# Optimization experiments

Measured on AMD Instinct MI355X. Metric: run time of the kernel, lower is better.

Reference implementation:

```python
import jax, jax.numpy as jnp
import numpy as np
import math

N_KM = [64, 16]  # part_nums_hierarchical
SPATIAL = 891    # 11*9*9, hardcoded in the original reshape


def _make_im2cluster(C, K, seed):
    # random assignment but guarantee >=2 members per cluster (original code
    # indexes zs[0] and skips singleton clusters, but would crash on empties)
    rng = np.random.RandomState(seed)
    base = np.repeat(np.arange(K), 2)
    rest = rng.randint(0, K, size=C - base.size)
    return np.concatenate([base, rest]).astype(np.int64)


def setup_inputs() -> dict:
    key = jax.random.key(0)
    conv_features = jax.random.normal(key, (8, 4096, 11, 9, 9), dtype=jnp.float32)
    im2cluster_0 = jnp.asarray(_make_im2cluster(4096, 64, 1))
    im2cluster_1 = jnp.asarray(_make_im2cluster(4096, 16, 2))
    return {"conv_features": conv_features,
            "im2cluster_0": im2cluster_0,
            "im2cluster_1": im2cluster_1}


def _safe_norm(diff):
    # row-wise L2 norm, grad-safe at exactly-zero rows (row 0 is zs[0]-zs[0])
    sq = jnp.sum(diff * diff, axis=1)
    return jnp.where(sq > 0, jnp.sqrt(jnp.where(sq > 0, sq, 1.0)), 0.0)


def _hpro_loss(conv_features, im2clusters):
    bs, C = conv_features.shape[0], conv_features.shape[1]
    D = SPATIAL * bs
    x = conv_features.reshape(bs, C, SPATIAL)
    loss = jnp.float32(0.0)
    loss_node = jnp.float32(0.0)
    for m, K in enumerate(N_KM):
        im2c = np.asarray(im2clusters[m])  # constant indices -> concrete group sizes
        zs_m, conc_m = [], []
        for c in range(K):
            idx = np.nonzero(im2c == c)[0]
            # faithful torch reshape: [bs, n_c, 891] -> [n_c, 891*bs] (row-major)
            zs = x[:, idx, :].reshape(-1, D)
            n_c = zs.shape[0]
            norm_sum = jnp.sum(_safe_norm(zs - zs[0]))
            conc_m.append(norm_sum / (n_c * math.log(n_c + 10)))
            zs_m.append(zs)
        rs = jnp.stack([z[0] for z in zs_m], axis=1)  # [D, K] first-member reps
        for c in range(K):
            u1 = zs_m[c]
            if u1.shape[0] == 1:
                continue
            nom = jnp.sum(u1 * u1[0], axis=1) / conc_m[c]                     # [n_c]
            den = jax.scipy.special.logsumexp((u1 @ rs) / conc_m[c], axis=1)  # [n_c]
            loss = loss + (-(nom - den)).mean()
        if m == 0:
            loss_node = loss
    return loss_node / C, (loss - loss_node) / (len(N_KM) * C)


def reference(conv_features, im2cluster_0, im2cluster_1):
    return _hpro_loss(conv_features, [im2cluster_0, im2cluster_1])
```

## Files before the change

### kernel.cpp

```cpp
#include <hip/hip_runtime.h>
#include <math.h>

#define CCH 4096
#define SP 891

typedef __attribute__((ext_vector_type(8))) short short8;
typedef __attribute__((ext_vector_type(4))) float f32x4;

__device__ __forceinline__ unsigned int pack_bf2(float a, float b) {
  unsigned int ua = __builtin_bit_cast(unsigned int, a);
  unsigned int ub = __builtin_bit_cast(unsigned int, b);
  ua = (ua + 0x7fffu + ((ua >> 16) & 1u)) >> 16;
  ub = (ub + 0x7fffu + ((ub >> 16) & 1u)) >> 16;
  return ua | (ub << 16);
}

__global__ void k_setup(const int* __restrict__ im0, const int* __restrict__ im1,
                        int* cnt0, int* off0, int* cnt1, int* off1,
                        int* mem0, int* mem1, int* rs0, int* rs1) {
  int cb = blockIdx.x;
  int level = (cb >= 64) ? 1 : 0;
  int c = level ? cb - 64 : cb;
  const int* im = level ? im1 : im0;
  int* members = level ? mem1 : mem0;
  int* rs = level ? rs1 : rs0;
  int lane = threadIdx.x;
  int lt = 0;
  for (int ch = lane; ch < CCH; ch += 64) lt += (im[ch] < c) ? 1 : 0;
  for (int o = 32; o; o >>= 1) lt += __shfl_xor(lt, o, 64);
  int base = lt;
  int cnt = 0;
  for (int chunk = 0; chunk < CCH; chunk += 64) {
    int ch = chunk + lane;
    bool m = (im[ch] == c);
    unsigned long long mk = __ballot(m);
    int pos = __popcll(mk & ((1ull << lane) - 1ull));
    if (m) members[base + cnt + pos] = ch;
    cnt += __popcll(mk);
  }
  int n = cnt;
  if (lane == 0) {
    if (level) { cnt1[c] = n; off1[c] = base; }
    else       { cnt0[c] = n; off0[c] = base; }
  }
  __syncthreads();
  for (int r = lane; r < n; r += 64) {
    #pragma unroll
    for (int q = 0; q < 8; q++) {
      int p = 8 * r + q;
      int b = p / n, j = p - b * n;
      rs[(size_t)(base + r) * 8 + q] = b * CCH + members[base + j];
    }
  }
}

__global__ void k_brep(const float* __restrict__ X,
    const int* __restrict__ off0, const int* __restrict__ off1,
    const int* __restrict__ rs0, const int* __restrict__ rs1,
    uint4* __restrict__ Bfrag0, uint4* __restrict__ Bfrag1) {
  int gid = blockIdx.x * 4 + (threadIdx.x >> 6);
  int l = threadIdx.x & 63;
  int lrow = l & 15, hi = l >> 4;
  int level = (gid >= 32) ? 1 : 0;
  int q = level ? (gid - 32) : (gid >> 2);
  int ct = level ? 0 : (gid & 3);
  int cc = ct * 16 + lrow;
  int base = level ? off1[cc] : off0[cc];
  int sid = (level ? rs1 : rs0)[(size_t)base * 8 + q];
  const float* ap = X + (size_t)sid * SP + hi * 8;
  uint4* dst = (level ? Bfrag1 + (size_t)(q * 28) * 64
                      : Bfrag0 + (size_t)((q * 4 + ct) * 28) * 64) + l;
  #pragma unroll 3
  for (int kc = 0; kc < 27; kc++) {
    float4 fa0 = *(const float4*)(ap + kc * 32);
    float4 fa1 = *(const float4*)(ap + kc * 32 + 4);
    uint4 ua;
    ua.x = pack_bf2(fa0.x, fa0.y); ua.y = pack_bf2(fa0.z, fa0.w);
    ua.z = pack_bf2(fa1.x, fa1.y); ua.w = pack_bf2(fa1.z, fa1.w);
    dst[kc * 64] = ua;
  }
  {
    float4 fa0, fa1;
    if (hi == 3) {
      fa0 = make_float4(ap[864], ap[865], ap[866], 0.f);
      fa1 = make_float4(0.f, 0.f, 0.f, 0.f);
    } else {
      fa0 = *(const float4*)(ap + 864);
      fa1 = *(const float4*)(ap + 868);
    }
    uint4 ua;
    ua.x = pack_bf2(fa0.x, fa0.y); ua.y = pack_bf2(fa0.z, fa0.w);
    ua.z = pack_bf2(fa1.x, fa1.y); ua.w = pack_bf2(fa1.z, fa1.w);
    dst[27 * 64] = ua;
  }
}

__global__ __launch_bounds__(256) void k_gemm_all(const float* __restrict__ X,
    const int* __restrict__ rs0, const int* __restrict__ rs1,
    const uint4* __restrict__ Bfrag0, const uint4* __restrict__ Bfrag1,
    float* __restrict__ P8_0, float* __restrict__ P8_1, float* __restrict__ sn2) {
  const int q = blockIdx.y, tid = threadIdx.x;
  const int l = tid & 63, w = tid >> 6;
  const int lrow = l & 15, hi = l >> 4;
  if (blockIdx.x < 128) {
    const int wm = w & 1, wn = w >> 1;
    const int rowTile = blockIdx.x * 2 + wm;
    const int sid = rs0[(size_t)(rowTile * 16 + lrow) * 8 + q];
    const float* ap = X + (size_t)sid * SP + hi * 8;
    const uint4* bq0 = Bfrag0 + (size_t)((q * 4 + wn * 2) * 28) * 64 + l;
    const uint4* bq1 = Bfrag0 + (size_t)((q * 4 + wn * 2 + 1) * 28) * 64 + l;
    f32x4 acc0 = {0.f, 0.f, 0.f, 0.f}, acc1 = {0.f, 0.f, 0.f, 0.f};
    float s2 = 0.f;
    #pragma unroll 3
    for (int kc = 0; kc < 27; kc++) {
      float4 fa0 = *(const float4*)(ap + kc * 32);
      float4 fa1 = *(const float4*)(ap + kc * 32 + 4);
      uint4 ub0 = bq0[kc * 64];
      uint4 ub1 = bq1[kc * 64];
      uint4 ua;
      ua.x = pack_bf2(fa0.x, fa0.y); ua.y = pack_bf2(fa0.z, fa0.w);
      ua.z = pack_bf2(fa1.x, fa1.y); ua.w = pack_bf2(fa1.z, fa1.w);
      s2 += fa0.x * fa0.x + fa0.y * fa0.y + fa0.z * fa0.z + fa0.w * fa0.w
          + fa1.x * fa1.x + fa1.y * fa1.y + fa1.z * fa1.z + fa1.w * fa1.w;
      short8 a = __builtin_bit_cast(short8, ua);
      acc0 = __builtin_amdgcn_mfma_f32_16x16x32_bf16(a, __builtin_bit_cast(short8, ub0), acc0, 0, 0, 0);
      acc1 = __builtin_amdgcn_mfma_f32_16x16x32_bf16(a, __builtin_bit_cast(short8, ub1), acc1, 0, 0, 0);
    }
    {
      float4 fa0, fa1;
      if (hi == 3) {
        fa0 = make_float4(ap[864], ap[865], ap[866], 0.f);
        fa1 = make_float4(0.f, 0.f, 0.f, 0.f);
      } else {
        fa0 = *(const float4*)(ap + 864);
        fa1 = *(const float4*)(ap + 868);
      }
      uint4 ub0 = bq0[27 * 64];
      uint4 ub1 = bq1[27 * 64];
      uint4 ua;
      ua.x = pack_bf2(fa0.x, fa0.y); ua.y = pack_bf2(fa0.z, fa0.w);
      ua.z = pack_bf2(fa1.x, fa1.y); ua.w = pack_bf2(fa1.z, fa1.w);
      s2 += fa0.x * fa0.x + fa0.y * fa0.y + fa0.z * fa0.z + fa0.w * fa0.w
          + fa1.x * fa1.x + fa1.y * fa1.y + fa1.z * fa1.z + fa1.w * fa1.w;
      short8 a = __builtin_bit_cast(short8, ua);
      acc0 = __builtin_amdgcn_mfma_f32_16x16x32_bf16(a, __builtin_bit_cast(short8, ub0), acc0, 0, 0, 0);
      acc1 = __builtin_amdgcn_mfma_f32_16x16x32_bf16(a, __builtin_bit_cast(short8, ub1), acc1, 0, 0, 0);
    }
    #pragma unroll
    for (int r = 0; r < 4; r++) {
      int row = rowTile * 16 + hi * 4 + r;
      float* dst = P8_0 + ((size_t)q * CCH + row) * 64;
      dst[wn * 32 + lrow] = acc0[r];
      dst[wn * 32 + 16 + lrow] = acc1[r];
    }
    s2 += __shfl_xor(s2, 16, 64);
    s2 += __shfl_xor(s2, 32, 64);
    if (wn == 0 && hi == 0) sn2[sid] = s2;
  } else {
    const int bx = blockIdx.x - 128;
    const int rowTile = bx * 4 + w;
    const int sid = rs1[(size_t)(rowTile * 16 + lrow) * 8 + q];
    const float* ap = X + (size_t)sid * SP + hi * 8;
    const uint4* bq = Bfrag1 + (size_t)(q * 28) * 64 + l;
    f32x4 acc = {0.f, 0.f, 0.f, 0.f};
    #pragma unroll 3
    for (int kc = 0; kc < 27; kc++) {
      float4 fa0 = *(const float4*)(ap + kc * 32);
      float4 fa1 = *(const float4*)(ap + kc * 32 + 4);
      uint4 ub = bq[kc * 64];
      uint4 ua;
      ua.x = pack_bf2(fa0.x, fa0.y); ua.y = pack_bf2(fa0.z, fa0.w);
      ua.z = pack_bf2(fa1.x, fa1.y); ua.w = pack_bf2(fa1.z, fa1.w);
      acc = __builtin_amdgcn_mfma_f32_16x16x32_bf16(
          __builtin_bit_cast(short8, ua), __builtin_bit_cast(short8, ub), acc, 0, 0, 0);
    }
    {
      float4 fa0, fa1;
      if (hi == 3) {
        fa0 = make_float4(ap[864], ap[865], ap[866], 0.f);
        fa1 = make_float4(0.f, 0.f, 0.f, 0.f);
      } else {
        fa0 = *(const float4*)(ap + 864);
        fa1 = *(const float4*)(ap + 868);
      }
      uint4 ub = bq[27 * 64];
      uint4 ua;
      ua.x = pack_bf2(fa0.x, fa0.y); ua.y = pack_bf2(fa0.z, fa0.w);
      ua.z = pack_bf2(fa1.x, fa1.y); ua.w = pack_bf2(fa1.z, fa1.w);
      acc = __builtin_amdgcn_mfma_f32_16x16x32_bf16(
          __builtin_bit_cast(short8, ua), __builtin_bit_cast(short8, ub), acc, 0, 0, 0);
    }
    #pragma unroll
    for (int r = 0; r < 4; r++) {
      int row = rowTile * 16 + hi * 4 + r;
      P8_1[((size_t)q * CCH + row) * 16 + lrow] = acc[r];
    }
  }
}

template<int K>
__device__ __forceinline__ void fin_body(const float* __restrict__ P8,
    const float* __restrict__ sn2, const int* __restrict__ rs,
    const int* __restrict__ cnt, const int* __restrict__ off,
    double* __restrict__ clLoss, int c) {
  __shared__ float pcc[4096];
  __shared__ float red[256];
  __shared__ double redd[256];
  __shared__ float s_conc;
  const int n = cnt[c], base = off[c];
  const int tid = threadIdx.x;
  float rn0 = 0.f;
  #pragma unroll
  for (int qq = 0; qq < 8; qq++) rn0 += sn2[rs[(size_t)base * 8 + qq]];
  float t = 0.f;
  for (int r = tid; r < n; r += 256) {
    float pd = 0.f, rn = 0.f;
    #pragma unroll
    for (int qq = 0; qq < 8; qq++) {
      pd += P8[((size_t)qq * CCH + base + r) * K + c];
      rn += sn2[rs[(size_t)(base + r) * 8 + qq]];
    }
    pcc[r] = pd;
    if (r > 0) {
      float d2 = rn - 2.f * pd + rn0;
      t += (d2 > 0.f) ? sqrtf(d2) : 0.f;
    }
  }
  red[tid] = t; __syncthreads();
  for (int o = 128; o; o >>= 1) { if (tid < o) red[tid] += red[tid + o]; __syncthreads(); }
  if (tid == 0) s_conc = red[0] / ((float)n * logf((float)n + 10.f));
  __syncthreads();
  const float invc = 1.f / s_conc;
  const int wv = tid >> 6, lane = tid & 63;
  const int sub = (K == 64) ? 0 : (lane >> 4);
  const int cc = lane & (K - 1);
  constexpr int RPI = (K == 64) ? 4 : 16;
  double acc = 0.0;
  for (int r = wv * (RPI / 4) + sub; r < n; r += RPI) {
    float s = 0.f;
    #pragma unroll
    for (int qq = 0; qq < 8; qq++) s += P8[((size_t)qq * CCH + base + r) * K + cc];
    float lg = s * invc;
    float m = lg;
    #pragma unroll
    for (int o = K / 2; o; o >>= 1) m = fmaxf(m, __shfl_xor(m, o, K));
    float e = expf(lg - m);
    float se = e;
    #pragma unroll
    for (int o = K / 2; o; o >>= 1) se += __shfl_xor(se, o, K);
    if (cc == 0) acc += (double)(m + logf(se)) - (double)(pcc[r] * invc);
  }
  redd[tid] = acc; __syncthreads();
  for (int o = 128; o; o >>= 1) { if (tid < o) redd[tid] += redd[tid + o]; __syncthreads(); }
  if (tid == 0) clLoss[c] = redd[0] / (double)n;
}

__global__ __launch_bounds__(256) void k_fin_all(const float* __restrict__ P8_0,
    const float* __restrict__ P8_1, const float* __restrict__ sn2,
    const int* __restrict__ rs0, const int* __restrict__ rs1,
    const int* __restrict__ cnt0, const int* __restrict__ off0,
    const int* __restrict__ cnt1, const int* __restrict__ off1,
    double* __restrict__ cl0, double* __restrict__ cl1) {
  if (blockIdx.x < 64) fin_body<64>(P8_0, sn2, rs0, cnt0, off0, cl0, blockIdx.x);
  else                 fin_body<16>(P8_1, sn2, rs1, cnt1, off1, cl1, blockIdx.x - 64);
}

__global__ void k_final(const double* __restrict__ cl0, const double* __restrict__ cl1,
                        float* __restrict__ out) {
  if (threadIdx.x == 0) {
    double s0 = 0.0, s1 = 0.0;
    for (int i = 0; i < 64; i++) s0 += cl0[i];
    for (int i = 0; i < 16; i++) s1 += cl1[i];
    out[0] = (float)(s0 / 4096.0);
    out[1] = (float)(s1 / 8192.0);
  }
}

extern "C" void kernel_launch(void* const* d_in, const int* in_sizes, int n_in,
                              void* d_out, int out_size, void* d_ws, size_t ws_size,
                              hipStream_t stream) {
  const float* X = (const float*)d_in[0];
  const int* im0 = (const int*)d_in[1];
  const int* im1 = (const int*)d_in[2];
  float* out = (float*)d_out;

  char* w = (char*)d_ws;
  auto alloc = [&](size_t bytes) -> char* {
    char* p = w; w += (bytes + 255) & ~(size_t)255; return p;
  };
  int*    cnt0  = (int*)alloc(64 * 4);
  int*    off0  = (int*)alloc(64 * 4);
  int*    cnt1  = (int*)alloc(16 * 4);
  int*    off1  = (int*)alloc(16 * 4);
  int*    mem0  = (int*)alloc((size_t)CCH * 4);
  int*    mem1  = (int*)alloc((size_t)CCH * 4);
  int*    rs0   = (int*)alloc((size_t)CCH * 8 * 4);
  int*    rs1   = (int*)alloc((size_t)CCH * 8 * 4);
  float*  sn2   = (float*)alloc((size_t)8 * CCH * 4);
  uint4*  Bfrag0 = (uint4*)alloc((size_t)32 * 28 * 64 * 16);
  uint4*  Bfrag1 = (uint4*)alloc((size_t)8 * 28 * 64 * 16);
  float*  P8_0  = (float*)alloc((size_t)8 * CCH * 64 * 4);
  float*  P8_1  = (float*)alloc((size_t)8 * CCH * 16 * 4);
  double* cl0   = (double*)alloc(64 * 8);
  double* cl1   = (double*)alloc(16 * 8);

  k_setup<<<80, 64, 0, stream>>>(im0, im1, cnt0, off0, cnt1, off1, mem0, mem1, rs0, rs1);
  k_brep<<<10, 256, 0, stream>>>(X, off0, off1, rs0, rs1, Bfrag0, Bfrag1);
  k_gemm_all<<<dim3(192, 8), 256, 0, stream>>>(X, rs0, rs1, Bfrag0, Bfrag1, P8_0, P8_1, sn2);
  k_fin_all<<<80, 256, 0, stream>>>(P8_0, P8_1, sn2, rs0, rs1, cnt0, off0, cnt1, off1, cl0, cl1);
  k_final<<<1, 64, 0, stream>>>(cl0, cl1, out);
}
```

Before: 114.7 us.

## Pre-pack fp32 activations into bf16 MFMA fragments once for both GEMM levels

Adds a k_pack kernel that reads each 891-element row of X once, converts it to bf16 through shared memory, computes the squared norm, and writes MFMA-ready fragment layouts for both hierarchy levels, using a new inverse map from level-0 to level-1 row positions. Before this, the GEMM read and converted X separately for each level, with strided unaligned gathers. The GEMM now streams coalesced pre-packed fragments with a 6-deep register prefetch. In exchange it adds an extra kernel launch and a bf16 write-then-read round trip of about 58 MB of Y0/Y1 through global memory.

Result: slower. 126.1 us (+9.9%).

```diff
diff --git a/kernel.cpp b/kernel.cpp
--- a/kernel.cpp
+++ b/kernel.cpp
@@ -17,7 +17,7 @@
 
 __global__ void k_setup(const int* __restrict__ im0, const int* __restrict__ im1,
                         int* cnt0, int* off0, int* cnt1, int* off1,
-                        int* mem0, int* mem1, int* rs0, int* rs1) {
+                        int* mem0, int* mem1, int* rs0, int* rs1, int* inv1) {
   int cb = blockIdx.x;
   int level = (cb >= 64) ? 1 : 0;
   int c = level ? cb - 64 : cb;
@@ -49,7 +49,9 @@
     for (int q = 0; q < 8; q++) {
       int p = 8 * r + q;
       int b = p / n, j = p - b * n;
-      rs[(size_t)(base + r) * 8 + q] = b * CCH + members[base + j];
+      int sid = b * CCH + members[base + j];
+      rs[(size_t)(base + r) * 8 + q] = sid;
+      if (level) inv1[sid] = ((base + r) << 3) | q;
     }
   }
 }
@@ -95,56 +97,83 @@
   }
 }
 
-__global__ __launch_bounds__(256) void k_gemm_all(const float* __restrict__ X,
-    const int* __restrict__ rs0, const int* __restrict__ rs1,
+__global__ __launch_bounds__(256) void k_pack(const float* __restrict__ X,
+    const int* __restrict__ rs0, const int* __restrict__ inv1,
+    uint4* __restrict__ Y0, uint4* __restrict__ Y1, float* __restrict__ sn2) {
+  __shared__ unsigned short T[16][912];
+  __shared__ int s_sid[16];
+  __shared__ int s_inv[16];
+  const int rt0 = blockIdx.x, q = blockIdx.y, tid = threadIdx.x;
+  if (tid < 16) {
+    int sid = rs0[(size_t)(rt0 * 16 + tid) * 8 + q];
+    s_sid[tid] = sid;
+    s_inv[tid] = inv1[sid];
+  }
+  __syncthreads();
+  const int i = tid >> 4, j = tid & 15;
+  const float* sp = X + (size_t)s_sid[i] * SP;
+  float s2 = 0.f;
+  #pragma unroll
+  for (int kcc = 0; kcc < 14; kcc++) {
+    int e = kcc * 64 + j * 4;
+    float4 v;
+    if (kcc < 13 || j < 14)      v = *(const float4*)(sp + e);
+    else if (j == 14)            v = make_float4(sp[888], sp[889], sp[890], 0.f);
+    else                         v = make_float4(0.f, 0.f, 0.f, 0.f);
+    s2 += v.x * v.x + v.y * v.y + v.z * v.z + v.w * v.w;
+    uint2 u;
+    u.x = pack_bf2(v.x, v.y); u.y = pack_bf2(v.z, v.w);
+    *(uint2*)&T[i][e] = u;
+  }
+  s2 += __shfl_xor(s2, 1, 16); s2 += __shfl_xor(s2, 2, 16);
+  s2 += __shfl_xor(s2, 4, 16); s2 += __shfl_xor(s2, 8, 16);
+  if (j == 0) sn2[s_sid[i]] = s2;
+  __syncthreads();
+  uint4* y0 = Y0 + (size_t)((q * 256 + rt0) * 28) * 64;
+  #pragma unroll
+  for (int it = 0; it < 7; it++) {
+    int pos = it * 256 + tid;
+    int kc = pos >> 6, l = pos & 63;
+    int lrow = l & 15, hi = l >> 4;
+    y0[pos] = *(const uint4*)&T[lrow][kc * 32 + hi * 8];
+  }
+  #pragma unroll
+  for (int it = 0; it < 7; it++) {
+    int p = it * 256 + tid;
+    int si = p / 112, pp = p - si * 112;
+    int kc = pp >> 2, hi = pp & 3;
+    uint4 v = *(const uint4*)&T[si][kc * 32 + hi * 8];
+    int inv = s_inv[si];
+    int row1 = inv >> 3, q1 = inv & 7;
+    Y1[((size_t)q1 * CCH + row1) * 112 + pp] = v;
+  }
+}
+
+__global__ __launch_bounds__(256) void k_gemm_all(
+    const uint4* __restrict__ Y0, const uint4* __restrict__ Y1,
     const uint4* __restrict__ Bfrag0, const uint4* __restrict__ Bfrag1,
-    float* __restrict__ P8_0, float* __restrict__ P8_1, float* __restrict__ sn2) {
+    float* __restrict__ P8_0, float* __restrict__ P8_1) {
   const int q = blockIdx.y, tid = threadIdx.x;
   const int l = tid & 63, w = tid >> 6;
   const int lrow = l & 15, hi = l >> 4;
   if (blockIdx.x < 128) {
     const int wm = w & 1, wn = w >> 1;
     const int rowTile = blockIdx.x * 2 + wm;
-    const int sid = rs0[(size_t)(rowTile * 16 + lrow) * 8 + q];
-    const float* ap = X + (size_t)sid * SP + hi * 8;
-    const uint4* bq0 = Bfrag0 + (size_t)((q * 4 + wn * 2) * 28) * 64 + l;
-    const uint4* bq1 = Bfrag0 + (size_t)((q * 4 + wn * 2 + 1) * 28) * 64 + l;
+    const uint4* aB = Y0 + (size_t)((q * 256 + rowTile) * 28) * 64 + l;
+    const uint4* b0 = Bfrag0 + (size_t)((q * 4 + wn * 2) * 28) * 64 + l;
+    const uint4* b1 = b0 + 28 * 64;
     f32x4 acc0 = {0.f, 0.f, 0.f, 0.f}, acc1 = {0.f, 0.f, 0.f, 0.f};
-    float s2 = 0.f;
-    #pragma unroll 3
-    for (int kc = 0; kc < 27; kc++) {
-      float4 fa0 = *(const float4*)(ap + kc * 32);
-      float4 fa1 = *(const float4*)(ap + kc * 32 + 4);
-      uint4 ub0 = bq0[kc * 64];
-      uint4 ub1 = bq1[kc * 64];
-      uint4 ua;
-      ua.x = pack_bf2(fa0.x, fa0.y); ua.y = pack_bf2(fa0.z, fa0.w);
-      ua.z = pack_bf2(fa1.x, fa1.y); ua.w = pack_bf2(fa1.z, fa1.w);
-      s2 += fa0.x * fa0.x + fa0.y * fa0.y + fa0.z * fa0.z + fa0.w * fa0.w
-          + fa1.x * fa1.x + fa1.y * fa1.y + fa1.z * fa1.z + fa1.w * fa1.w;
-      short8 a = __builtin_bit_cast(short8, ua);
-      acc0 = __builtin_amdgcn_mfma_f32_16x16x32_bf16(a, __builtin_bit_cast(short8, ub0), acc0, 0, 0, 0);
-      acc1 = __builtin_amdgcn_mfma_f32_16x16x32_bf16(a, __builtin_bit_cast(short8, ub1), acc1, 0, 0, 0);
-    }
-    {
-      float4 fa0, fa1;
-      if (hi == 3) {
-        fa0 = make_float4(ap[864], ap[865], ap[866], 0.f);
-        fa1 = make_float4(0.f, 0.f, 0.f, 0.f);
-      } else {
-        fa0 = *(const float4*)(ap + 864);
-        fa1 = *(const float4*)(ap + 868);
-      }
-      uint4 ub0 = bq0[27 * 64];
-      uint4 ub1 = bq1[27 * 64];
-      uint4 ua;
-      ua.x = pack_bf2(fa0.x, fa0.y); ua.y = pack_bf2(fa0.z, fa0.w);
-      ua.z = pack_bf2(fa1.x, fa1.y); ua.w = pack_bf2(fa1.z, fa1.w);
-      s2 += fa0.x * fa0.x + fa0.y * fa0.y + fa0.z * fa0.z + fa0.w * fa0.w
-          + fa1.x * fa1.x + fa1.y * fa1.y + fa1.z * fa1.z + fa1.w * fa1.w;
-      short8 a = __builtin_bit_cast(short8, ua);
-      acc0 = __builtin_amdgcn_mfma_f32_16x16x32_bf16(a, __builtin_bit_cast(short8, ub0), acc0, 0, 0, 0);
-      acc1 = __builtin_amdgcn_mfma_f32_16x16x32_bf16(a, __builtin_bit_cast(short8, ub1), acc1, 0, 0, 0);
+    uint4 Ab[6], B0b[6], B1b[6];
+    #pragma unroll
+    for (int d = 0; d < 6; d++) { Ab[d] = aB[d * 64]; B0b[d] = b0[d * 64]; B1b[d] = b1[d * 64]; }
+    #pragma unroll
+    for (int kc = 0; kc < 28; kc++) {
+      int d = kc % 6;
+      short8 a8 = __builtin_bit_cast(short8, Ab[d]);
+      acc0 = __builtin_amdgcn_mfma_f32_16x16x32_bf16(a8, __builtin_bit_cast(short8, B0b[d]), acc0, 0, 0, 0);
+      acc1 = __builtin_amdgcn_mfma_f32_16x16x32_bf16(a8, __builtin_bit_cast(short8, B1b[d]), acc1, 0, 0, 0);
+      int nk = kc + 6;
+      if (nk < 28) { Ab[d] = aB[nk * 64]; B0b[d] = b0[nk * 64]; B1b[d] = b1[nk * 64]; }
     }
     #pragma unroll
     for (int r = 0; r < 4; r++) {
@@ -153,46 +182,26 @@
       dst[wn * 32 + lrow] = acc0[r];
       dst[wn * 32 + 16 + lrow] = acc1[r];
     }
-    s2 += __shfl_xor(s2, 16, 64);
-    s2 += __shfl_xor(s2, 32, 64);
-    if (wn == 0 && hi == 0) sn2[sid] = s2;
   } else {
     const int bx = blockIdx.x - 128;
-    const int rowTile = bx * 4 + w;
-    const int sid = rs1[(size_t)(rowTile * 16 + lrow) * 8 + q];
-    const float* ap = X + (size_t)sid * SP + hi * 8;
+    const int rt1 = bx * 4 + w;
+    const uint4* aB = Y1 + ((size_t)q * CCH + rt1 * 16 + lrow) * 112 + hi;
     const uint4* bq = Bfrag1 + (size_t)(q * 28) * 64 + l;
     f32x4 acc = {0.f, 0.f, 0.f, 0.f};
-    #pragma unroll 3
-    for (int kc = 0; kc < 27; kc++) {
-      float4 fa0 = *(const float4*)(ap + kc * 32);
-      float4 fa1 = *(const float4*)(ap + kc * 32 + 4);
-      uint4 ub = bq[kc * 64];
-      uint4 ua;
-      ua.x = pack_bf2(fa0.x, fa0.y); ua.y = pack_bf2(fa0.z, fa0.w);
-      ua.z = pack_bf2(fa1.x, fa1.y); ua.w = pack_bf2(fa1.z, fa1.w);
+    uint4 Ab[6], Bb[6];
+    #pragma unroll
+    for (int d = 0; d < 6; d++) { Ab[d] = aB[d * 4]; Bb[d] = bq[d * 64]; }
+    #pragma unroll
+    for (int kc = 0; kc < 28; kc++) {
+      int d = kc % 6;
       acc = __builtin_amdgcn_mfma_f32_16x16x32_bf16(
-          __builtin_bit_cast(short8, ua), __builtin_bit_cast(short8, ub), acc, 0, 0, 0);
-    }
-    {
-      float4 fa0, fa1;
-      if (hi == 3) {
-        fa0 = make_float4(ap[864], ap[865], ap[866], 0.f);
-        fa1 = make_float4(0.f, 0.f, 0.f, 0.f);
-      } else {
-        fa0 = *(const float4*)(ap + 864);
-        fa1 = *(const float4*)(ap + 868);
-      }
-      uint4 ub = bq[27 * 64];
-      uint4 ua;
-      ua.x = pack_bf2(fa0.x, fa0.y); ua.y = pack_bf2(fa0.z, fa0.w);
-      ua.z = pack_bf2(fa1.x, fa1.y); ua.w = pack_bf2(fa1.z, fa1.w);
-      acc = __builtin_amdgcn_mfma_f32_16x16x32_bf16(
-          __builtin_bit_cast(short8, ua), __builtin_bit_cast(short8, ub), acc, 0, 0, 0);
+          __builtin_bit_cast(short8, Ab[d]), __builtin_bit_cast(short8, Bb[d]), acc, 0, 0, 0);
+      int nk = kc + 6;
+      if (nk < 28) { Ab[d] = aB[nk * 4]; Bb[d] = bq[nk * 64]; }
     }
     #pragma unroll
     for (int r = 0; r < 4; r++) {
-      int row = rowTile * 16 + hi * 4 + r;
+      int row = rt1 * 16 + hi * 4 + r;
       P8_1[((size_t)q * CCH + row) * 16 + lrow] = acc[r];
     }
   }
@@ -296,17 +305,21 @@
   int*    mem1  = (int*)alloc((size_t)CCH * 4);
   int*    rs0   = (int*)alloc((size_t)CCH * 8 * 4);
   int*    rs1   = (int*)alloc((size_t)CCH * 8 * 4);
+  int*    inv1  = (int*)alloc((size_t)8 * CCH * 4);
   float*  sn2   = (float*)alloc((size_t)8 * CCH * 4);
   uint4*  Bfrag0 = (uint4*)alloc((size_t)32 * 28 * 64 * 16);
   uint4*  Bfrag1 = (uint4*)alloc((size_t)8 * 28 * 64 * 16);
+  uint4*  Y0    = (uint4*)alloc((size_t)8 * 256 * 28 * 64 * 16);
+  uint4*  Y1    = (uint4*)alloc((size_t)8 * CCH * 112 * 16);
   float*  P8_0  = (float*)alloc((size_t)8 * CCH * 64 * 4);
   float*  P8_1  = (float*)alloc((size_t)8 * CCH * 16 * 4);
   double* cl0   = (double*)alloc(64 * 8);
   double* cl1   = (double*)alloc(16 * 8);
 
-  k_setup<<<80, 64, 0, stream>>>(im0, im1, cnt0, off0, cnt1, off1, mem0, mem1, rs0, rs1);
+  k_setup<<<80, 64, 0, stream>>>(im0, im1, cnt0, off0, cnt1, off1, mem0, mem1, rs0, rs1, inv1);
   k_brep<<<10, 256, 0, stream>>>(X, off0, off1, rs0, rs1, Bfrag0, Bfrag1);
-  k_gemm_all<<<dim3(192, 8), 256, 0, stream>>>(X, rs0, rs1, Bfrag0, Bfrag1, P8_0, P8_1, sn2);
+  k_pack<<<dim3(256, 8), 256, 0, stream>>>(X, rs0, inv1, Y0, Y1, sn2);
+  k_gemm_all<<<dim3(192, 8), 256, 0, stream>>>(Y0, Y1, Bfrag0, Bfrag1, P8_0, P8_1);
   k_fin_all<<<80, 256, 0, stream>>>(P8_0, P8_1, sn2, rs0, rs1, cnt0, off0, cnt1, off1, cl0, cl1);
   k_final<<<1, 64, 0, stream>>>(cl0, cl1, out);
 }
```
